# Performance work log

Hardware: AMD Instinct MI355X
Metric: run time of the kernel (lower is better)

The kernel has to match this reference:

```python
import jax, jax.numpy as jnp
import numpy as np


def setup_inputs() -> dict:
    B, S, DK, DV, H = 2, 2048, 1024, 1024, 16
    ks = jax.random.split(jax.random.key(0), 7)
    keys = jax.random.normal(ks[0], (B, S, DK), jnp.float32)
    queries = jax.random.normal(ks[1], (B, S, DK), jnp.float32)
    values = jax.random.normal(ks[2], (B, S, DV), jnp.float32)
    # per-head projection weights, stored as [H, in, out] (torch Linear uses W.T; math-equivalent)
    WQ = jax.random.normal(ks[3], (H, DK, DK // H), jnp.float32) / np.sqrt(DK).astype(np.float32)
    WK = jax.random.normal(ks[4], (H, DK, DK // H), jnp.float32) / np.sqrt(DK).astype(np.float32)
    WV = jax.random.normal(ks[5], (H, DV, DV // H), jnp.float32) / np.sqrt(DV).astype(np.float32)
    WO = jax.random.normal(ks[6], (DV, DV), jnp.float32) / np.sqrt(DV).astype(np.float32)
    return {"keys": keys, "queries": queries, "values": values,
            "WQ": WQ, "WK": WK, "WV": WV, "WO": WO, "masking": 1}


def reference(keys, queries, values, WQ, WK, WV, WO, masking):
    B, Sq, _ = queries.shape
    Sk = keys.shape[1]
    # batched per-head projections (original loops over heads in Python)
    Q = jnp.einsum('bqd,hde->bhqe', queries, WQ)   # [B,H,Sq,dh]
    K = jnp.einsum('bkd,hde->bhke', keys, WK)      # [B,H,Sk,dh]
    V = jnp.einsum('bkd,hde->bhke', values, WV)    # [B,H,Sk,dvh]
    q_idx = jnp.arange(Sq)[:, None]
    k_idx = jnp.arange(Sk)[None, :]
    causal = k_idx <= q_idx
    # NOTE: original never applies the slope m; bias = (i - j) for i<=j else 0, same for all heads
    bias = jnp.where(causal, (k_idx - q_idx).astype(jnp.float32), 0.0)
    scale = np.float32(1.0 / np.sqrt(Sk))  # original divides by sqrt(keys.shape[1])
    y = (jnp.einsum('bhqe,bhke->bhqk', Q, K) + bias) * scale
    if masking:
        y = jnp.where(causal, y, -jnp.inf)
    # original: F.softmax(y, 1) on [B,Sq,Sk] -> softmax over the QUERY axis
    z = jax.nn.softmax(y, axis=2)
    out = jnp.einsum('bhqk,bhke->bhqe', z, V)      # [B,H,Sq,dvh]
    out = out.transpose(0, 2, 1, 3).reshape(B, Sq, -1)  # concat heads on last dim
    return out @ WO
```

## Files before the change

kernel.cpp:

```cpp
#include <hip/hip_runtime.h>
#include <math.h>

#define SEQ    2048
#define DMODEL 1024
#define NH     16
#define DH     64
#define NB     2
#define BHN    (NB*NH)

static constexpr float SCALE = 0.02209708691207961f;

typedef __attribute__((ext_vector_type(8))) short short8;
typedef __attribute__((ext_vector_type(4))) short short4v;
typedef __attribute__((ext_vector_type(4))) float f32x4;

__device__ __forceinline__ short f2bf(float f) {
    union { float f; unsigned u; } v; v.f = f;
    unsigned r = (v.u + 0x7FFFu + ((v.u >> 16) & 1u)) >> 16;
    return (short)r;
}

__device__ __forceinline__ unsigned pack_bf2(float a, float b) {
    union { float f; unsigned u; } ua, ub; ua.f = a; ub.f = b;
    return __builtin_amdgcn_perm(ub.u + 0x8000u, ua.u + 0x8000u, 0x07060302u);
}

__device__ __forceinline__ float bf2f(short s) {
    union { unsigned u; float f; } v; v.u = ((unsigned)(unsigned short)s) << 16;
    return v.f;
}

__device__ __forceinline__ void load16_lds(const short* g, short* l) {
    __builtin_amdgcn_global_load_lds(
        (const __attribute__((address_space(1))) unsigned int*)g,
        (__attribute__((address_space(3))) unsigned int*)l,
        16, 0, 0);
}

__device__ __forceinline__ void stage_rows(const short* g, short* s, int t, int ldg, int nIter) {
    int wave = t >> 6, lane = t & 63;
    #pragma unroll
    for (int i = 0; i < 4; ++i) {
        if (i >= nIter) break;
        int E   = i * 2048 + wave * 512 + lane * 8;
        int row = E >> 6;
        int blk = (lane & 7) ^ (row & 7);
        load16_lds(g + (size_t)row * ldg + blk * 8, s + i * 2048 + wave * 512);
    }
}

__device__ __forceinline__ short8 frag_sw(const short* s, int rowbase, int ks, int lane) {
    int m   = rowbase + (lane & 15);
    int q   = lane >> 4;
    int blk = (ks * 4 + q) ^ (m & 7);
    return *(const short8*)(s + m * 64 + blk * 8);
}

__global__ __launch_bounds__(256) void convert_x(
    const float* __restrict__ q, const float* __restrict__ k, const float* __restrict__ v,
    short* __restrict__ Xq, short* __restrict__ Xk, short* __restrict__ Xv)
{
    const int z = blockIdx.z;
    const float* src = (z == 0) ? q : (z == 1) ? k : v;
    short* dst = (z == 0) ? Xq : (z == 1) ? Xk : Xv;
    size_t idx = ((size_t)blockIdx.x * 256 + threadIdx.x) * 8;
    float4 a = *(const float4*)(src + idx);
    float4 b = *(const float4*)(src + idx + 4);
    short8 o;
    o[0] = f2bf(a.x); o[1] = f2bf(a.y); o[2] = f2bf(a.z); o[3] = f2bf(a.w);
    o[4] = f2bf(b.x); o[5] = f2bf(b.y); o[6] = f2bf(b.z); o[7] = f2bf(b.w);
    *(short8*)(dst + idx) = o;
}

__global__ __launch_bounds__(256) void convert_w(
    const float* __restrict__ WQ, const float* __restrict__ WK,
    const float* __restrict__ WV, const float* __restrict__ WO,
    short* __restrict__ WQt, short* __restrict__ WKt,
    short* __restrict__ WVt, short* __restrict__ WOt)
{
    const int z = blockIdx.z;
    const int k0 = blockIdx.x * 64;
    const int ny = blockIdx.y;
    const float* W = (z == 0) ? WQ : (z == 1) ? WK : (z == 2) ? WV : WO;
    short* Wt = (z == 0) ? WQt : (z == 1) ? WKt : (z == 2) ? WVt : WOt;

    __shared__ float Ts[64][68];
    const int t = threadIdx.x;
    const int tr = t >> 4, tc4 = (t & 15) * 4;

    #pragma unroll
    for (int i = 0; i < 4; ++i) {
        int row = tr + i * 16;
        float4 v;
        if (z < 3) v = *(const float4*)(W + (size_t)ny * DMODEL * DH + (size_t)(k0 + row) * DH + tc4);
        else       v = *(const float4*)(W + (size_t)(k0 + row) * DMODEL + ny * 64 + tc4);
        Ts[tc4 + 0][row] = v.x; Ts[tc4 + 1][row] = v.y;
        Ts[tc4 + 2][row] = v.z; Ts[tc4 + 3][row] = v.w;
    }
    __syncthreads();
    #pragma unroll
    for (int i = 0; i < 4; ++i) {
        int nl = tr + i * 16;
        short4v o;
        o[0] = f2bf(Ts[nl][tc4 + 0]); o[1] = f2bf(Ts[nl][tc4 + 1]);
        o[2] = f2bf(Ts[nl][tc4 + 2]); o[3] = f2bf(Ts[nl][tc4 + 3]);
        *(short4v*)(Wt + (size_t)(ny * 64 + nl) * DMODEL + k0 + tc4) = o;
    }
}

__global__ __launch_bounds__(256) void gemm_nt(
    const short* __restrict__ A0, const short* __restrict__ A1, const short* __restrict__ A2,
    const short* __restrict__ B0, const short* __restrict__ B1, const short* __restrict__ B2,
    short* __restrict__ Y0, short* __restrict__ Y1, short* __restrict__ Y2)
{
    const int z = blockIdx.z;
    const short* X  = (z == 0) ? A0 : (z == 1) ? A1 : A2;
    const short* Wt = (z == 0) ? B0 : (z == 1) ? B1 : B2;
    short* Y        = (z == 0) ? Y0 : (z == 1) ? Y1 : Y2;
    const bool vOrient = (z == 2);

    const int lin = blockIdx.y * 8 + blockIdx.x;
    const int n0 = (lin >> 5) * 128;
    const int m0 = (lin & 31) * 128;

    __shared__ short As[128 * 64];
    __shared__ short Bs[128 * 64];

    const int t = threadIdx.x;
    const int wave = t >> 6, lane = t & 63;
    const int wrow = (wave >> 1) * 64, wcol = (wave & 1) * 64;
    const int quad = lane >> 4, l15 = lane & 15;

    f32x4 acc[4][4];
    #pragma unroll
    for (int i = 0; i < 4; ++i)
        #pragma unroll
        for (int j = 0; j < 4; ++j)
            acc[i][j] = (f32x4)0.f;

    for (int k0 = 0; k0 < DMODEL; k0 += 64) {
        __syncthreads();
        stage_rows(X  + (size_t)m0 * DMODEL + k0, As, t, DMODEL, 4);
        stage_rows(Wt + (size_t)n0 * DMODEL + k0, Bs, t, DMODEL, 4);
        __syncthreads();
        if (!vOrient) {
            #pragma unroll
            for (int ks = 0; ks < 2; ++ks) {
                short8 xf[4], wf[4];
                #pragma unroll
                for (int i = 0; i < 4; ++i) xf[i] = frag_sw(As, wrow + i * 16, ks, lane);
                #pragma unroll
                for (int i = 0; i < 4; ++i) wf[i] = frag_sw(Bs, wcol + i * 16, ks, lane);
                #pragma unroll
                for (int a = 0; a < 4; ++a)
                    #pragma unroll
                    for (int b = 0; b < 4; ++b)
                        acc[a][b] = __builtin_amdgcn_mfma_f32_16x16x32_bf16(
                            wf[a], xf[b], acc[a][b], 0, 0, 0);
            }
        } else {
            #pragma unroll
            for (int ks = 0; ks < 2; ++ks) {
                short8 xf[4], wf[4];
                #pragma unroll
                for (int i = 0; i < 4; ++i) xf[i] = frag_sw(As, wrow + i * 16, ks, lane);
                #pragma unroll
                for (int i = 0; i < 4; ++i) wf[i] = frag_sw(Bs, wcol + i * 16, ks, lane);
                #pragma unroll
                for (int a = 0; a < 4; ++a)
                    #pragma unroll
                    for (int b = 0; b < 4; ++b)
                        acc[a][b] = __builtin_amdgcn_mfma_f32_16x16x32_bf16(
                            xf[a], wf[b], acc[a][b], 0, 0, 0);
            }
        }
    }

    if (vOrient) {
        #pragma unroll
        for (int a = 0; a < 4; ++a) {
            #pragma unroll
            for (int b = 0; b < 4; ++b) {
                int m = m0 + wrow + a * 16 + quad * 4;
                int n = n0 + wcol + b * 16 + l15;
                int bb = m >> 11, s = m & 2047, h = n >> 6, e = n & 63;
                short4v o;
                #pragma unroll
                for (int i = 0; i < 4; ++i) o[i] = f2bf(acc[a][b][i]);
                *(short4v*)(Y + ((size_t)((bb * NH + h) * DH + e)) * SEQ + s) = o;
            }
        }
    } else {
        #pragma unroll
        for (int a = 0; a < 4; ++a) {
            #pragma unroll
            for (int b = 0; b < 4; ++b) {
                int n = n0 + wcol + a * 16 + quad * 4;
                int m = m0 + wrow + b * 16 + l15;
                int bb = m >> 11, s = m & 2047, h = n >> 6, e = n & 63;
                short4v o;
                #pragma unroll
                for (int i = 0; i < 4; ++i) o[i] = f2bf(acc[a][b][i]);
                *(short4v*)(Y + ((size_t)((bb * NH + h) * SEQ + s)) * DH + e) = o;
            }
        }
    }
}

__global__ __launch_bounds__(256) void gemm_out(
    const short* __restrict__ X, const short* __restrict__ Wt,
    float* __restrict__ o0, float* __restrict__ o1)
{
    const int z = blockIdx.z;
    const int lin = blockIdx.y * 8 + blockIdx.x;
    const int n0 = (lin >> 5) * 128;
    const int m0 = (lin & 31) * 128;

    __shared__ short As[2][128 * 64];
    __shared__ short Bs[2][128 * 64];

    const int t = threadIdx.x;
    const int wave = t >> 6, lane = t & 63;
    const int wrow = (wave >> 1) * 64, wcol = (wave & 1) * 64;
    const int quad = lane >> 4, l15 = lane & 15;

    f32x4 acc[4][4];
    #pragma unroll
    for (int i = 0; i < 4; ++i)
        #pragma unroll
        for (int j = 0; j < 4; ++j)
            acc[i][j] = (f32x4)0.f;

    const int kBeg = z * 512;
    stage_rows(X  + (size_t)m0 * DMODEL + kBeg, As[0], t, DMODEL, 4);
    stage_rows(Wt + (size_t)n0 * DMODEL + kBeg, Bs[0], t, DMODEL, 4);
    __syncthreads();

    int cur = 0;
    for (int it = 0; it < 8; ++it) {
        if (it + 1 < 8) {
            const int k0 = kBeg + (it + 1) * 64;
            stage_rows(X  + (size_t)m0 * DMODEL + k0, As[cur ^ 1], t, DMODEL, 4);
            stage_rows(Wt + (size_t)n0 * DMODEL + k0, Bs[cur ^ 1], t, DMODEL, 4);
        }
        #pragma unroll
        for (int ks = 0; ks < 2; ++ks) {
            short8 xf[4], wf[4];
            #pragma unroll
            for (int i = 0; i < 4; ++i) xf[i] = frag_sw(As[cur], wrow + i * 16, ks, lane);
            #pragma unroll
            for (int i = 0; i < 4; ++i) wf[i] = frag_sw(Bs[cur], wcol + i * 16, ks, lane);
            #pragma unroll
            for (int a = 0; a < 4; ++a)
                #pragma unroll
                for (int b = 0; b < 4; ++b)
                    acc[a][b] = __builtin_amdgcn_mfma_f32_16x16x32_bf16(
                        wf[a], xf[b], acc[a][b], 0, 0, 0);
        }
        __syncthreads();
        cur ^= 1;
    }

    float* dst = z ? o1 : o0;
    #pragma unroll
    for (int a = 0; a < 4; ++a) {
        #pragma unroll
        for (int b = 0; b < 4; ++b) {
            int n = n0 + wcol + a * 16 + quad * 4;
            int m = m0 + wrow + b * 16 + l15;
            float4 o = make_float4(acc[a][b][0], acc[a][b][1], acc[a][b][2], acc[a][b][3]);
            *(float4*)(dst + (size_t)m * DMODEL + n) = o;
        }
    }
}

__global__ __launch_bounds__(256) void reduce_add(
    float* __restrict__ dst, const float* __restrict__ src)
{
    size_t i = ((size_t)blockIdx.x * 256 + threadIdx.x) * 8;
    float4 a0 = *(float4*)(dst + i);
    float4 a1 = *(float4*)(dst + i + 4);
    float4 b0 = *(const float4*)(src + i);
    float4 b1 = *(const float4*)(src + i + 4);
    a0.x += b0.x; a0.y += b0.y; a0.z += b0.z; a0.w += b0.w;
    a1.x += b1.x; a1.y += b1.y; a1.z += b1.z; a1.w += b1.w;
    *(float4*)(dst + i) = a0;
    *(float4*)(dst + i + 4) = a1;
}

__global__ __launch_bounds__(256) void stats_mfma(
    const short* __restrict__ Qg, const short* __restrict__ Kg,
    float* __restrict__ rDg, const int* __restrict__ mask_p)
{
    const int gblk = blockIdx.x;
    const int masking = mask_p[0];

    __shared__ short Ks[64 * 64];
    __shared__ short Qs[2][128 * 64];

    const int t = threadIdx.x;
    const int wave = t >> 6, lane = t & 63;
    const int quad = lane >> 4, l15 = lane & 15;

    for (int item = 0; item < 2; ++item) {
        const int w  = item ? (1023 - gblk) : gblk;
        const int kt = w >> 5, bh = w & 31;
        const int k0 = kt * 64;

        const int qb0 = masking ? (kt >> 1) : 0;
        const int q0s = qb0 * 128;
        if (item) __syncthreads();
        stage_rows(Kg + ((size_t)bh * SEQ + k0) * DH, Ks, t, DH, 2);
        stage_rows(Qg + ((size_t)bh * SEQ + q0s) * DH, Qs[0], t, DH, 4);
        __syncthreads();

        short8 Kf[2];
        Kf[0] = frag_sw(Ks, wave * 16, 0, lane);
        Kf[1] = frag_sw(Ks, wave * 16, 1, lane);

        int   kgi[4];
        float biasK[4];
        #pragma unroll
        for (int i = 0; i < 4; ++i) {
            kgi[i] = k0 + wave * 16 + quad * 4 + i;
            biasK[i] = SCALE * (float)kgi[i];
        }
        float qS[8];
        #pragma unroll
        for (int nt = 0; nt < 8; ++nt)
            qS[nt] = SCALE * (float)(q0s + nt * 16 + l15);

        float dsum[4] = {0.f, 0.f, 0.f, 0.f};
        const int nIter = masking ? (16 - qb0) : 16;
        for (int it = 0; it < nIter; ++it) {
            const int cur = it & 1;
            if (it > 0) __syncthreads();
            if (it + 1 < nIter)
                stage_rows(Qg + ((size_t)bh * SEQ + q0s + (it + 1) * 128) * DH, Qs[1 - cur], t, DH, 4);

            f32x4 acc[8];
            #pragma unroll
            for (int nt = 0; nt < 8; ++nt) acc[nt] = (f32x4)0.f;
            __builtin_amdgcn_s_setprio(1);
            #pragma unroll
            for (int ks = 0; ks < 2; ++ks)
                #pragma unroll
                for (int nt = 0; nt < 8; ++nt)
                    acc[nt] = __builtin_amdgcn_mfma_f32_16x16x32_bf16(
                        Kf[ks], frag_sw(Qs[cur], nt * 16, ks, lane), acc[nt], 0, 0, 0);
            __builtin_amdgcn_s_setprio(0);

            const bool exact = masking && (it == 0);
            #pragma unroll
            for (int nt = 0; nt < 8; ++nt) {
                #pragma unroll
                for (int i = 0; i < 4; ++i) {
                    float diff = biasK[i] - qS[nt];
                    float v = masking ? fmaf(acc[nt][i], SCALE, diff)
                                      : fmaf(acc[nt][i], SCALE, fminf(diff, 0.f));
                    float e = __expf(v);
                    if (exact)
                        e = (kgi[i] <= (q0s + nt * 16 + l15)) ? e : 0.f;
                    dsum[i] += e;
                }
            }
            #pragma unroll
            for (int nt = 0; nt < 8; ++nt) qS[nt] += 128.f * SCALE;
        }

        #pragma unroll
        for (int i = 0; i < 4; ++i) {
            float d = dsum[i];
            #pragma unroll
            for (int mm = 1; mm < 16; mm <<= 1) d += __shfl_xor(d, mm);
            dsum[i] = d;
        }
        if (l15 == 0) {
            const int kc = k0 + wave * 16 + quad * 4;
            float4 o = make_float4(1.f / dsum[0], 1.f / dsum[1], 1.f / dsum[2], 1.f / dsum[3]);
            *(float4*)(rDg + (size_t)bh * SEQ + kc) = o;
        }
    }
}

template<int MODE>
__device__ __forceinline__ void attn_tile(
    const short* Kbuf, const short* Vbuf, short* Pw,
    const short8 Qf[2], const float bias[4][4], f32x4 oacc[4],
    const float* __restrict__ rDk,
    int lane, int quad, int l15, int qloc)
{
    f32x4 sacc[4];
    #pragma unroll
    for (int mt = 0; mt < 4; ++mt) sacc[mt] = (f32x4)0.f;
    __builtin_amdgcn_s_setprio(1);
    #pragma unroll
    for (int ks = 0; ks < 2; ++ks) {
        #pragma unroll
        for (int mt = 0; mt < 4; ++mt)
            sacc[mt] = __builtin_amdgcn_mfma_f32_16x16x32_bf16(
                frag_sw(Kbuf, mt * 16, ks, lane), Qf[ks], sacc[mt], 0, 0, 0);
    }
    __builtin_amdgcn_s_setprio(0);
    __asm__ volatile("" ::: "memory");
    #pragma unroll
    for (int mt = 0; mt < 4; ++mt) {
        float4 rv4 = *(const float4*)(rDk + mt * 16 + quad * 4);
        float rv[4] = {rv4.x, rv4.y, rv4.z, rv4.w};
        float p[4];
        #pragma unroll
        for (int i = 0; i < 4; ++i) {
            float bi = bias[mt][i];
            float v = (MODE == 2) ? fmaf(sacc[mt][i], SCALE, fminf(bi, 0.f))
                                  : fmaf(sacc[mt][i], SCALE, bi);
            float e = __expf(v);
            if (MODE == 1)
                e = ((mt * 16 + quad * 4 + i) <= qloc) ? e : 0.f;
            p[i] = e * rv[i];
        }
        int blk = (2 * mt + (quad >> 1)) ^ (l15 & 7);
        *(uint2*)(Pw + l15 * 64 + blk * 8 + (quad & 1) * 4) =
            make_uint2(pack_bf2(p[0], p[1]), pack_bf2(p[2], p[3]));
    }
    __asm__ volatile("" ::: "memory");
    __builtin_amdgcn_s_setprio(1);
    #pragma unroll
    for (int ks = 0; ks < 2; ++ks) {
        short8 pf = *(const short8*)(Pw + l15 * 64 + (((ks * 4 + quad) ^ (l15 & 7)) * 8));
        #pragma unroll
        for (int mt = 0; mt < 4; ++mt)
            oacc[mt] = __builtin_amdgcn_mfma_f32_16x16x32_bf16(
                frag_sw(Vbuf, mt * 16, ks, lane), pf, oacc[mt], 0, 0, 0);
    }
    __builtin_amdgcn_s_setprio(0);
}

__global__ __launch_bounds__(256) void attn_mfma(
    const short* __restrict__ Qg, const short* __restrict__ Kg, const short* __restrict__ Vt,
    const float* __restrict__ rDg, short* __restrict__ attnb, const int* __restrict__ mask_p)
{
    const int gblk = blockIdx.x;
    const int masking = mask_p[0];

    __shared__ short Qs[64 * 64];
    __shared__ short Ks[2][64 * 64];
    __shared__ short Vts[2][64 * 64];

    const int t = threadIdx.x;
    const int wave = t >> 6, lane = t & 63;
    const int quad = lane >> 4, l15 = lane & 15;
    short* Pw = Qs + wave * 1024;
    const int qloc = wave * 16 + l15;

    for (int item = 0; item < 2; ++item) {
        const int w  = item ? (1023 - gblk) : gblk;
        const int qt = w >> 5, bh = w & 31;
        const int b = bh >> 4, h = bh & (NH - 1);
        const int q0 = qt * 64;
        const float* rDb = rDg + (size_t)bh * SEQ;

        if (item) __syncthreads();
        stage_rows(Qg + ((size_t)bh * SEQ + q0) * DH, Qs, t, DH, 2);
        stage_rows(Kg + (size_t)bh * SEQ * DH, Ks[0], t, DH, 2);
        stage_rows(Vt + (size_t)bh * DH * SEQ, Vts[0], t, SEQ, 2);
        __syncthreads();

        short8 Qf[2];
        Qf[0] = frag_sw(Qs, wave * 16, 0, lane);
        Qf[1] = frag_sw(Qs, wave * 16, 1, lane);

        float bias[4][4];
        #pragma unroll
        for (int mt = 0; mt < 4; ++mt)
            #pragma unroll
            for (int i = 0; i < 4; ++i)
                bias[mt][i] = SCALE * (float)((mt * 16 + quad * 4 + i)
                                            - (q0 + qloc));

        f32x4 oacc[4];
        #pragma unroll
        for (int mt = 0; mt < 4; ++mt) oacc[mt] = (f32x4)0.f;

        const int nIter = masking ? (qt + 1) : (SEQ / 64);
        for (int it = 0; it < nIter; ++it) {
            const int cur = it & 1;
            if (it > 0) __syncthreads();
            if (it + 1 < nIter) {
                const int k0n = (it + 1) * 64;
                stage_rows(Kg + ((size_t)bh * SEQ + k0n) * DH, Ks[1 - cur], t, DH, 2);
                stage_rows(Vt + (size_t)bh * DH * SEQ + k0n, Vts[1 - cur], t, SEQ, 2);
            }
            const float* rDk = rDb + it * 64;
            if (!masking)       attn_tile<2>(Ks[cur], Vts[cur], Pw, Qf, bias, oacc, rDk, lane, quad, l15, qloc);
            else if (it == qt)  attn_tile<1>(Ks[cur], Vts[cur], Pw, Qf, bias, oacc, rDk, lane, quad, l15, qloc);
            else                attn_tile<0>(Ks[cur], Vts[cur], Pw, Qf, bias, oacc, rDk, lane, quad, l15, qloc);
            #pragma unroll
            for (int mt = 0; mt < 4; ++mt)
                #pragma unroll
                for (int i = 0; i < 4; ++i)
                    bias[mt][i] += 64.f * SCALE;
        }

        #pragma unroll
        for (int mt = 0; mt < 4; ++mt) {
            int e = mt * 16 + quad * 4;
            int q = q0 + wave * 16 + l15;
            short4v o;
            #pragma unroll
            for (int i = 0; i < 4; ++i) o[i] = f2bf(oacc[mt][i]);
            *(short4v*)(attnb + ((size_t)(b * SEQ + q)) * DMODEL + h * DH + e) = o;
        }
    }
}

extern "C" void kernel_launch(void* const* d_in, const int* in_sizes, int n_in,
                              void* d_out, int out_size, void* d_ws, size_t ws_size,
                              hipStream_t stream) {
    const float* keys    = (const float*)d_in[0];
    const float* queries = (const float*)d_in[1];
    const float* values  = (const float*)d_in[2];
    const float* WQ      = (const float*)d_in[3];
    const float* WK      = (const float*)d_in[4];
    const float* WV      = (const float*)d_in[5];
    const float* WO      = (const float*)d_in[6];
    const int*   mask_p  = (const int*)d_in[7];
    float* out = (float*)d_out;

    const size_t nX = (size_t)NB * SEQ * DMODEL;
    const size_t nW = (size_t)DMODEL * DMODEL;
    const size_t nQ = (size_t)BHN * SEQ * DH;

    short* ws = (short*)d_ws;
    short* Xq    = ws;
    short* Xk    = Xq + nX;
    short* Xv    = Xk + nX;
    short* WQt   = Xv + nX;
    short* WKt   = WQt + nW;
    short* WVt   = WKt + nW;
    short* WOt   = WVt + nW;
    short* Qg    = WOt + nW;
    short* Kg    = Qg + nQ;
    short* Vtg   = Kg + nQ;
    short* attnb = Vtg + nQ;
    float* rDg   = (float*)(attnb + nX);
    float* outP1 = (float*)ws;

    convert_x<<<dim3(2048, 1, 3), dim3(256), 0, stream>>>(queries, keys, values, Xq, Xk, Xv);
    convert_w<<<dim3(16, 16, 4), dim3(256), 0, stream>>>(WQ, WK, WV, WO, WQt, WKt, WVt, WOt);
    gemm_nt<<<dim3(8, 32, 3), dim3(256), 0, stream>>>(
        Xq, Xk, Xv, WQt, WKt, WVt, Qg, Kg, Vtg);
    stats_mfma<<<dim3(512), dim3(256), 0, stream>>>(Qg, Kg, rDg, mask_p);
    attn_mfma<<<dim3(512), dim3(256), 0, stream>>>(Qg, Kg, Vtg, rDg, attnb, mask_p);
    gemm_out<<<dim3(8, 32, 2), dim3(256), 0, stream>>>(attnb, WOt, out, outP1);
    reduce_add<<<dim3(2048), dim3(256), 0, stream>>>(out, outP1);
}
```

Baseline: 257.8 us.

## Fold softmax reciprocal denominators into V and merge conversion kernels

Since the softmax runs over the query axis, each key column has one normaliser. The stats kernel now multiplies the transposed V rows by that reciprocal in place, so the attention kernel no longer loads rD or multiplies each probability by it. The two fp32-to-bf16 conversion kernels are also merged into a single launch to save a launch. In exchange, V is read and written once more in global memory and is rounded to bf16 a second time after scaling, which adds a little precision error.

```diff
diff --git a/kernel.cpp b/kernel.cpp
--- a/kernel.cpp
+++ b/kernel.cpp
@@ -56,46 +56,48 @@
     return *(const short8*)(s + m * 64 + blk * 8);
 }
 
-__global__ __launch_bounds__(256) void convert_x(
+__global__ __launch_bounds__(256) void convert_all(
     const float* __restrict__ q, const float* __restrict__ k, const float* __restrict__ v,
-    short* __restrict__ Xq, short* __restrict__ Xk, short* __restrict__ Xv)
-{
-    const int z = blockIdx.z;
-    const float* src = (z == 0) ? q : (z == 1) ? k : v;
-    short* dst = (z == 0) ? Xq : (z == 1) ? Xk : Xv;
-    size_t idx = ((size_t)blockIdx.x * 256 + threadIdx.x) * 8;
-    float4 a = *(const float4*)(src + idx);
-    float4 b = *(const float4*)(src + idx + 4);
-    short8 o;
-    o[0] = f2bf(a.x); o[1] = f2bf(a.y); o[2] = f2bf(a.z); o[3] = f2bf(a.w);
-    o[4] = f2bf(b.x); o[5] = f2bf(b.y); o[6] = f2bf(b.z); o[7] = f2bf(b.w);
-    *(short8*)(dst + idx) = o;
-}
-
-__global__ __launch_bounds__(256) void convert_w(
+    short* __restrict__ Xq, short* __restrict__ Xk, short* __restrict__ Xv,
     const float* __restrict__ WQ, const float* __restrict__ WK,
     const float* __restrict__ WV, const float* __restrict__ WO,
     short* __restrict__ WQt, short* __restrict__ WKt,
     short* __restrict__ WVt, short* __restrict__ WOt)
 {
-    const int z = blockIdx.z;
-    const int k0 = blockIdx.x * 64;
-    const int ny = blockIdx.y;
+    __shared__ float Ts[64][68];
+    const int lin = blockIdx.x;
+    const int t = threadIdx.x;
+
+    if (lin < 6144) {
+        const int z = lin / 2048, bx = lin - z * 2048;
+        const float* src = (z == 0) ? q : (z == 1) ? k : v;
+        short* dst = (z == 0) ? Xq : (z == 1) ? Xk : Xv;
+        size_t idx = ((size_t)bx * 256 + t) * 8;
+        float4 a = *(const float4*)(src + idx);
+        float4 b = *(const float4*)(src + idx + 4);
+        short8 o;
+        o[0] = f2bf(a.x); o[1] = f2bf(a.y); o[2] = f2bf(a.z); o[3] = f2bf(a.w);
+        o[4] = f2bf(b.x); o[5] = f2bf(b.y); o[6] = f2bf(b.z); o[7] = f2bf(b.w);
+        *(short8*)(dst + idx) = o;
+        return;
+    }
+
+    const int wl = lin - 6144;
+    const int z = wl >> 8, rem = wl & 255;
+    const int k0 = (rem & 15) * 64;
+    const int ny = rem >> 4;
     const float* W = (z == 0) ? WQ : (z == 1) ? WK : (z == 2) ? WV : WO;
     short* Wt = (z == 0) ? WQt : (z == 1) ? WKt : (z == 2) ? WVt : WOt;
 
-    __shared__ float Ts[64][68];
-    const int t = threadIdx.x;
     const int tr = t >> 4, tc4 = (t & 15) * 4;
-
     #pragma unroll
     for (int i = 0; i < 4; ++i) {
         int row = tr + i * 16;
-        float4 v;
-        if (z < 3) v = *(const float4*)(W + (size_t)ny * DMODEL * DH + (size_t)(k0 + row) * DH + tc4);
-        else       v = *(const float4*)(W + (size_t)(k0 + row) * DMODEL + ny * 64 + tc4);
-        Ts[tc4 + 0][row] = v.x; Ts[tc4 + 1][row] = v.y;
-        Ts[tc4 + 2][row] = v.z; Ts[tc4 + 3][row] = v.w;
+        float4 v4;
+        if (z < 3) v4 = *(const float4*)(W + (size_t)ny * DMODEL * DH + (size_t)(k0 + row) * DH + tc4);
+        else       v4 = *(const float4*)(W + (size_t)(k0 + row) * DMODEL + ny * 64 + tc4);
+        Ts[tc4 + 0][row] = v4.x; Ts[tc4 + 1][row] = v4.y;
+        Ts[tc4 + 2][row] = v4.z; Ts[tc4 + 3][row] = v4.w;
     }
     __syncthreads();
     #pragma unroll
@@ -290,13 +292,14 @@
 
 __global__ __launch_bounds__(256) void stats_mfma(
     const short* __restrict__ Qg, const short* __restrict__ Kg,
-    float* __restrict__ rDg, const int* __restrict__ mask_p)
+    short* __restrict__ Vt, const int* __restrict__ mask_p)
 {
     const int gblk = blockIdx.x;
     const int masking = mask_p[0];
 
     __shared__ short Ks[64 * 64];
     __shared__ short Qs[2][128 * 64];
+    __shared__ float rsh[64];
 
     const int t = threadIdx.x;
     const int wave = t >> 6, lane = t & 63;
@@ -376,10 +379,27 @@
             dsum[i] = d;
         }
         if (l15 == 0) {
-            const int kc = k0 + wave * 16 + quad * 4;
-            float4 o = make_float4(1.f / dsum[0], 1.f / dsum[1], 1.f / dsum[2], 1.f / dsum[3]);
-            *(float4*)(rDg + (size_t)bh * SEQ + kc) = o;
-        }
+            #pragma unroll
+            for (int i = 0; i < 4; ++i)
+                rsh[wave * 16 + quad * 4 + i] = 1.f / dsum[i];
+        }
+        __syncthreads();
+
+        short* Vs = Vt + (size_t)bh * DH * SEQ + k0;
+        const int e  = t >> 2;
+        const int sc = (t & 3) * 16;
+        short8 v0 = *(short8*)(Vs + (size_t)e * SEQ + sc);
+        short8 v1 = *(short8*)(Vs + (size_t)e * SEQ + sc + 8);
+        union { unsigned u[4]; short8 s8; } o0, o1;
+        #pragma unroll
+        for (int j = 0; j < 4; ++j) {
+            o0.u[j] = pack_bf2(bf2f(v0[2 * j])     * rsh[sc + 2 * j],
+                               bf2f(v0[2 * j + 1]) * rsh[sc + 2 * j + 1]);
+            o1.u[j] = pack_bf2(bf2f(v1[2 * j])     * rsh[sc + 8 + 2 * j],
+                               bf2f(v1[2 * j + 1]) * rsh[sc + 8 + 2 * j + 1]);
+        }
+        *(short8*)(Vs + (size_t)e * SEQ + sc)     = o0.s8;
+        *(short8*)(Vs + (size_t)e * SEQ + sc + 8) = o1.s8;
     }
 }
 
@@ -387,7 +407,6 @@
 __device__ __forceinline__ void attn_tile(
     const short* Kbuf, const short* Vbuf, short* Pw,
     const short8 Qf[2], const float bias[4][4], f32x4 oacc[4],
-    const float* __restrict__ rDk,
     int lane, int quad, int l15, int qloc)
 {
     f32x4 sacc[4];
@@ -405,8 +424,6 @@
     __asm__ volatile("" ::: "memory");
     #pragma unroll
     for (int mt = 0; mt < 4; ++mt) {
-        float4 rv4 = *(const float4*)(rDk + mt * 16 + quad * 4);
-        float rv[4] = {rv4.x, rv4.y, rv4.z, rv4.w};
         float p[4];
         #pragma unroll
         for (int i = 0; i < 4; ++i) {
@@ -416,7 +433,7 @@
             float e = __expf(v);
             if (MODE == 1)
                 e = ((mt * 16 + quad * 4 + i) <= qloc) ? e : 0.f;
-            p[i] = e * rv[i];
+            p[i] = e;
         }
         int blk = (2 * mt + (quad >> 1)) ^ (l15 & 7);
         *(uint2*)(Pw + l15 * 64 + blk * 8 + (quad & 1) * 4) =
@@ -437,7 +454,7 @@
 
 __global__ __launch_bounds__(256) void attn_mfma(
     const short* __restrict__ Qg, const short* __restrict__ Kg, const short* __restrict__ Vt,
-    const float* __restrict__ rDg, short* __restrict__ attnb, const int* __restrict__ mask_p)
+    short* __restrict__ attnb, const int* __restrict__ mask_p)
 {
     const int gblk = blockIdx.x;
     const int masking = mask_p[0];
@@ -457,7 +474,6 @@
         const int qt = w >> 5, bh = w & 31;
         const int b = bh >> 4, h = bh & (NH - 1);
         const int q0 = qt * 64;
-        const float* rDb = rDg + (size_t)bh * SEQ;
 
         if (item) __syncthreads();
         stage_rows(Qg + ((size_t)bh * SEQ + q0) * DH, Qs, t, DH, 2);
@@ -490,10 +506,9 @@
                 stage_rows(Kg + ((size_t)bh * SEQ + k0n) * DH, Ks[1 - cur], t, DH, 2);
                 stage_rows(Vt + (size_t)bh * DH * SEQ + k0n, Vts[1 - cur], t, SEQ, 2);
             }
-            const float* rDk = rDb + it * 64;
-            if (!masking)       attn_tile<2>(Ks[cur], Vts[cur], Pw, Qf, bias, oacc, rDk, lane, quad, l15, qloc);
-            else if (it == qt)  attn_tile<1>(Ks[cur], Vts[cur], Pw, Qf, bias, oacc, rDk, lane, quad, l15, qloc);
-            else                attn_tile<0>(Ks[cur], Vts[cur], Pw, Qf, bias, oacc, rDk, lane, quad, l15, qloc);
+            if (!masking)       attn_tile<2>(Ks[cur], Vts[cur], Pw, Qf, bias, oacc, lane, quad, l15, qloc);
+            else if (it == qt)  attn_tile<1>(Ks[cur], Vts[cur], Pw, Qf, bias, oacc, lane, quad, l15, qloc);
+            else                attn_tile<0>(Ks[cur], Vts[cur], Pw, Qf, bias, oacc, lane, quad, l15, qloc);
             #pragma unroll
             for (int mt = 0; mt < 4; ++mt)
                 #pragma unroll
@@ -542,15 +557,15 @@
     short* Kg    = Qg + nQ;
     short* Vtg   = Kg + nQ;
     short* attnb = Vtg + nQ;
-    float* rDg   = (float*)(attnb + nX);
     float* outP1 = (float*)ws;
 
-    convert_x<<<dim3(2048, 1, 3), dim3(256), 0, stream>>>(queries, keys, values, Xq, Xk, Xv);
-    convert_w<<<dim3(16, 16, 4), dim3(256), 0, stream>>>(WQ, WK, WV, WO, WQt, WKt, WVt, WOt);
+    convert_all<<<dim3(7168), dim3(256), 0, stream>>>(
+        queries, keys, values, Xq, Xk, Xv,
+        WQ, WK, WV, WO, WQt, WKt, WVt, WOt);
     gemm_nt<<<dim3(8, 32, 3), dim3(256), 0, stream>>>(
         Xq, Xk, Xv, WQt, WKt, WVt, Qg, Kg, Vtg);
-    stats_mfma<<<dim3(512), dim3(256), 0, stream>>>(Qg, Kg, rDg, mask_p);
-    attn_mfma<<<dim3(512), dim3(256), 0, stream>>>(Qg, Kg, Vtg, rDg, attnb, mask_p);
+    stats_mfma<<<dim3(512), dim3(256), 0, stream>>>(Qg, Kg, Vtg, mask_p);
+    attn_mfma<<<dim3(512), dim3(256), 0, stream>>>(Qg, Kg, Vtg, attnb, mask_p);
     gemm_out<<<dim3(8, 32, 2), dim3(256), 0, stream>>>(attnb, WOt, out, outP1);
     reduce_add<<<dim3(2048), dim3(256), 0, stream>>>(out, outP1);
 }
```

After: 253.1 us. About the same (-1.8%).
